# Optimization experiments

Hardware: AMD Instinct MI355X
Metric: run time of the kernel (lower is better)

The kernel has to match this reference:

```python
import jax, jax.numpy as jnp
import numpy as np

IN_FEATURES_A = 256
IN_FEATURES_B = 256


def setup_inputs() -> dict:
    key = jax.random.key(0)
    # x: [2, batch, features]; x[0] -> x_a, x[1] -> x_b
    x = jax.random.normal(key, (2, 2048, 256), dtype=jnp.float32)
    return {"x": x}


def reference(x) -> jnp.ndarray:
    # Split and truncate exactly like the torch module
    x_a = x[0][:, :IN_FEATURES_A]  # [B, A]
    x_b = x[1][:, :IN_FEATURES_B]  # [B, Kb]
    bsz = x_a.shape[0]
    # torch.kron of two 1-D vectors == flattened outer product (a-major order)
    y = jnp.einsum("ba,bk->bak", x_a, x_b).reshape(bsz, IN_FEATURES_A * IN_FEATURES_B)
    return jax.nn.softmax(y, axis=1)
```

## Files before the change

### kernel.cpp

```cpp
#include <hip/hip_runtime.h>


constexpr int FA   = 256;
constexpr int FB   = 256;
constexpr int ROWS = 2048;
constexpr int RPB  = 4;
constexpr float LOG2E = 1.4426950408889634f;

typedef float f32x4 __attribute__((ext_vector_type(4)));

__global__ __launch_bounds__(256) void krone_softmax_kernel(
    const float* __restrict__ x, float* __restrict__ out) {
  const int tid  = threadIdx.x;
  const int wid  = tid >> 6;
  const int lane = tid & 63;
  const int j    = lane * 4;
  const int row0 = blockIdx.x * RPB;

  __shared__ float sa[FA];
  __shared__ float wred[4][4];
  __shared__ float wsum[4];

  for (int r = 0; r < RPB; ++r) {
    const int row = row0 + r;
    const float* __restrict__ xa = x + (size_t)row * FA;
    const float* __restrict__ xb = x + (size_t)ROWS * FA + (size_t)row * FB;

    const float a = xa[tid];
    const float b = xb[tid];
    f32x4 b4 = *reinterpret_cast<const f32x4*>(&xb[j]);
    __syncthreads();
    sa[tid] = a;

    float maxa = a, mina = a, maxb = b, minb = b;
#pragma unroll
    for (int off = 32; off > 0; off >>= 1) {
      maxa = fmaxf(maxa, __shfl_xor(maxa, off));
      mina = fminf(mina, __shfl_xor(mina, off));
      maxb = fmaxf(maxb, __shfl_xor(maxb, off));
      minb = fminf(minb, __shfl_xor(minb, off));
    }
    if (lane == 0) {
      wred[wid][0] = maxa; wred[wid][1] = mina;
      wred[wid][2] = maxb; wred[wid][3] = minb;
    }
    __syncthreads();
    const float MA = fmaxf(fmaxf(wred[0][0], wred[1][0]), fmaxf(wred[2][0], wred[3][0]));
    const float mA = fminf(fminf(wred[0][1], wred[1][1]), fminf(wred[2][1], wred[3][1]));
    const float MB = fmaxf(fmaxf(wred[0][2], wred[1][2]), fmaxf(wred[2][2], wred[3][2]));
    const float mB = fminf(fminf(wred[0][3], wred[1][3]), fminf(wred[2][3], wred[3][3]));
    const float M = fmaxf(fmaxf(MA * MB, MA * mB), fmaxf(mA * MB, mA * mB));
    const float mM2 = -M * LOG2E;

    const float bs = b * LOG2E;
    float s0 = 0.f, s1 = 0.f, s2 = 0.f, s3 = 0.f;
#pragma unroll 4
    for (int i = 0; i < FA; i += 4) {
      s0 += __builtin_amdgcn_exp2f(fmaf(sa[i + 0], bs, mM2));
      s1 += __builtin_amdgcn_exp2f(fmaf(sa[i + 1], bs, mM2));
      s2 += __builtin_amdgcn_exp2f(fmaf(sa[i + 2], bs, mM2));
      s3 += __builtin_amdgcn_exp2f(fmaf(sa[i + 3], bs, mM2));
    }
    float s = (s0 + s1) + (s2 + s3);
#pragma unroll
    for (int off = 32; off > 0; off >>= 1) s += __shfl_xor(s, off);
    if (lane == 0) wsum[wid] = s;
    __syncthreads();
    const float sum = (wsum[0] + wsum[1]) + (wsum[2] + wsum[3]);

    const float C = mM2 - __builtin_amdgcn_logf(sum);

    f32x4 b4s = b4 * LOG2E;
    float* __restrict__ oseg =
        out + (size_t)row * (FA * FB) + wid * (64 * FB);
#pragma unroll 8
    for (int it = 0; it < 64; ++it) {
      const float av = sa[wid * 64 + it];
      f32x4 v;
      v.x = __builtin_amdgcn_exp2f(fmaf(av, b4s.x, C));
      v.y = __builtin_amdgcn_exp2f(fmaf(av, b4s.y, C));
      v.z = __builtin_amdgcn_exp2f(fmaf(av, b4s.z, C));
      v.w = __builtin_amdgcn_exp2f(fmaf(av, b4s.w, C));
      __builtin_nontemporal_store(v, reinterpret_cast<f32x4*>(&oseg[it * FB + j]));
    }
  }
}

extern "C" void kernel_launch(void* const* d_in, const int* in_sizes, int n_in,
                              void* d_out, int out_size, void* d_ws, size_t ws_size,
                              hipStream_t stream) {
  const float* x = (const float*)d_in[0];
  float* out = (float*)d_out;
  krone_softmax_kernel<<<ROWS / RPB, 256, 0, stream>>>(x, out);
}
```

Baseline: 109.4 us.

## Interleave next row's softmax denominator with current row's output stores

Each block now handles two rows. The exp-sum for the second row is computed inside the store loop of the first row, so the exp work can hide behind the memory-bound write stream. Shared-memory staging of x_a is replaced with wave shuffles, and each wave computes the global min/max redundantly, which removes a block barrier. The cost is more register pressure, more shuffle instructions, and half as many rows per block, which doubles the grid size.

```diff
diff --git a/kernel.cpp b/kernel.cpp
--- a/kernel.cpp
+++ b/kernel.cpp
@@ -4,85 +4,122 @@
 constexpr int FA   = 256;
 constexpr int FB   = 256;
 constexpr int ROWS = 2048;
-constexpr int RPB  = 4;
+constexpr int RPB  = 2;
 constexpr float LOG2E = 1.4426950408889634f;
 
 typedef float f32x4 __attribute__((ext_vector_type(4)));
 
-__global__ __launch_bounds__(256) void krone_softmax_kernel(
+__global__ __launch_bounds__(256) void krone_pipe_kernel(
     const float* __restrict__ x, float* __restrict__ out) {
   const int tid  = threadIdx.x;
   const int wid  = tid >> 6;
   const int lane = tid & 63;
-  const int j    = lane * 4;
   const int row0 = blockIdx.x * RPB;
 
-  __shared__ float sa[FA];
-  __shared__ float wred[4][4];
   __shared__ float wsum[4];
 
-  for (int r = 0; r < RPB; ++r) {
-    const int row = row0 + r;
-    const float* __restrict__ xa = x + (size_t)row * FA;
-    const float* __restrict__ xb = x + (size_t)ROWS * FA + (size_t)row * FB;
+  const float* __restrict__ xa0 = x + (size_t)row0 * FA;
+  const float* __restrict__ xb0 = x + (size_t)ROWS * FA + (size_t)row0 * FB;
+  const float* __restrict__ xa1 = xa0 + FA;
+  const float* __restrict__ xb1 = xb0 + FB;
 
-    const float a = xa[tid];
-    const float b = xb[tid];
-    f32x4 b4 = *reinterpret_cast<const f32x4*>(&xb[j]);
-    __syncthreads();
-    sa[tid] = a;
+  const float ar0 = xa0[lane], ar1 = xa0[64 + lane];
+  const float ar2 = xa0[128 + lane], ar3 = xa0[192 + lane];
+  const float aw  = xa0[wid * 64 + lane];
+  f32x4 b4        = *(const f32x4*)&xb0[lane * 4];
+  const float bc  = xb0[wid * 64 + lane];
+  const float nr0 = xa1[lane], nr1 = xa1[64 + lane];
+  const float nr2 = xa1[128 + lane], nr3 = xa1[192 + lane];
+  const float naw = xa1[wid * 64 + lane];
+  f32x4 nb4       = *(const f32x4*)&xb1[lane * 4];
+  const float nbc = xb1[wid * 64 + lane];
 
-    float maxa = a, mina = a, maxb = b, minb = b;
+#define MINMAX_M(A0, A1, A2, A3, B4, OUTM)                                    \
+  {                                                                           \
+    float mxa = fmaxf(fmaxf(A0, A1), fmaxf(A2, A3));                          \
+    float mna = fminf(fminf(A0, A1), fminf(A2, A3));                          \
+    float mxb = fmaxf(fmaxf(B4.x, B4.y), fmaxf(B4.z, B4.w));                  \
+    float mnb = fminf(fminf(B4.x, B4.y), fminf(B4.z, B4.w));                  \
+    _Pragma("unroll")                                                         \
+    for (int off = 32; off > 0; off >>= 1) {                                  \
+      mxa = fmaxf(mxa, __shfl_xor(mxa, off));                                 \
+      mna = fminf(mna, __shfl_xor(mna, off));                                 \
+      mxb = fmaxf(mxb, __shfl_xor(mxb, off));                                 \
+      mnb = fminf(mnb, __shfl_xor(mnb, off));                                 \
+    }                                                                         \
+    OUTM = fmaxf(fmaxf(mxa * mxb, mxa * mnb), fmaxf(mna * mxb, mna * mnb));   \
+  }
+
+  float M0; MINMAX_M(ar0, ar1, ar2, ar3, b4, M0);
+  const float mM2_0 = -M0 * LOG2E;
+  float M1; MINMAX_M(nr0, nr1, nr2, nr3, nb4, M1);
+  const float mM2_1 = -M1 * LOG2E;
+#undef MINMAX_M
+
+  const float bs0 = bc * LOG2E;
+  float a0 = 0.f, a1 = 0.f, a2 = 0.f, a3 = 0.f;
+#define DEN64(REG)                                                            \
+  _Pragma("unroll")                                                           \
+  for (int m = 0; m < 64; m += 4) {                                           \
+    a0 += __builtin_amdgcn_exp2f(fmaf(__shfl(REG, m + 0), bs0, mM2_0));       \
+    a1 += __builtin_amdgcn_exp2f(fmaf(__shfl(REG, m + 1), bs0, mM2_0));       \
+    a2 += __builtin_amdgcn_exp2f(fmaf(__shfl(REG, m + 2), bs0, mM2_0));       \
+    a3 += __builtin_amdgcn_exp2f(fmaf(__shfl(REG, m + 3), bs0, mM2_0));       \
+  }
+  DEN64(ar0) DEN64(ar1) DEN64(ar2) DEN64(ar3)
+#undef DEN64
+  float part = (a0 + a1) + (a2 + a3);
 #pragma unroll
-    for (int off = 32; off > 0; off >>= 1) {
-      maxa = fmaxf(maxa, __shfl_xor(maxa, off));
-      mina = fminf(mina, __shfl_xor(mina, off));
-      maxb = fmaxf(maxb, __shfl_xor(maxb, off));
-      minb = fminf(minb, __shfl_xor(minb, off));
-    }
-    if (lane == 0) {
-      wred[wid][0] = maxa; wred[wid][1] = mina;
-      wred[wid][2] = maxb; wred[wid][3] = minb;
-    }
-    __syncthreads();
-    const float MA = fmaxf(fmaxf(wred[0][0], wred[1][0]), fmaxf(wred[2][0], wred[3][0]));
-    const float mA = fminf(fminf(wred[0][1], wred[1][1]), fminf(wred[2][1], wred[3][1]));
-    const float MB = fmaxf(fmaxf(wred[0][2], wred[1][2]), fmaxf(wred[2][2], wred[3][2]));
-    const float mB = fminf(fminf(wred[0][3], wred[1][3]), fminf(wred[2][3], wred[3][3]));
-    const float M = fmaxf(fmaxf(MA * MB, MA * mB), fmaxf(mA * MB, mA * mB));
-    const float mM2 = -M * LOG2E;
+  for (int off = 32; off > 0; off >>= 1) part += __shfl_xor(part, off);
+  if (lane == 0) wsum[wid] = part;
+  __syncthreads();
+  const float sum0 = (wsum[0] + wsum[1]) + (wsum[2] + wsum[3]);
+  const float C0 = mM2_0 - __builtin_amdgcn_logf(sum0);
+  __syncthreads();
 
-    const float bs = b * LOG2E;
-    float s0 = 0.f, s1 = 0.f, s2 = 0.f, s3 = 0.f;
-#pragma unroll 4
-    for (int i = 0; i < FA; i += 4) {
-      s0 += __builtin_amdgcn_exp2f(fmaf(sa[i + 0], bs, mM2));
-      s1 += __builtin_amdgcn_exp2f(fmaf(sa[i + 1], bs, mM2));
-      s2 += __builtin_amdgcn_exp2f(fmaf(sa[i + 2], bs, mM2));
-      s3 += __builtin_amdgcn_exp2f(fmaf(sa[i + 3], bs, mM2));
-    }
-    float s = (s0 + s1) + (s2 + s3);
+  const f32x4 b4s = b4 * LOG2E;
+  const float bsn = nbc * LOG2E;
+  float* __restrict__ oseg0 = out + (size_t)row0 * (FA * FB) + wid * (64 * FB);
+  float d0 = 0.f, d1 = 0.f, d2 = 0.f, d3 = 0.f;
+#define SUBBLK(S, NREG)                                                       \
+  _Pragma("unroll")                                                           \
+  for (int k = 0; k < 16; ++k) {                                              \
+    const int it = 16 * (S) + k;                                              \
+    const float av = __shfl(aw, it);                                          \
+    f32x4 v;                                                                  \
+    v.x = __builtin_amdgcn_exp2f(fmaf(av, b4s.x, C0));                        \
+    v.y = __builtin_amdgcn_exp2f(fmaf(av, b4s.y, C0));                        \
+    v.z = __builtin_amdgcn_exp2f(fmaf(av, b4s.z, C0));                        \
+    v.w = __builtin_amdgcn_exp2f(fmaf(av, b4s.w, C0));                        \
+    __builtin_nontemporal_store(v, (f32x4*)&oseg0[it * FB + lane * 4]);       \
+    d0 += __builtin_amdgcn_exp2f(fmaf(__shfl(NREG, 4 * k + 0), bsn, mM2_1));  \
+    d1 += __builtin_amdgcn_exp2f(fmaf(__shfl(NREG, 4 * k + 1), bsn, mM2_1));  \
+    d2 += __builtin_amdgcn_exp2f(fmaf(__shfl(NREG, 4 * k + 2), bsn, mM2_1));  \
+    d3 += __builtin_amdgcn_exp2f(fmaf(__shfl(NREG, 4 * k + 3), bsn, mM2_1));  \
+  }
+  SUBBLK(0, nr0) SUBBLK(1, nr1) SUBBLK(2, nr2) SUBBLK(3, nr3)
+#undef SUBBLK
+
+  float partn = (d0 + d1) + (d2 + d3);
 #pragma unroll
-    for (int off = 32; off > 0; off >>= 1) s += __shfl_xor(s, off);
-    if (lane == 0) wsum[wid] = s;
-    __syncthreads();
-    const float sum = (wsum[0] + wsum[1]) + (wsum[2] + wsum[3]);
+  for (int off = 32; off > 0; off >>= 1) partn += __shfl_xor(partn, off);
+  if (lane == 0) wsum[wid] = partn;
+  __syncthreads();
+  const float sum1 = (wsum[0] + wsum[1]) + (wsum[2] + wsum[3]);
+  const float C1 = mM2_1 - __builtin_amdgcn_logf(sum1);
 
-    const float C = mM2 - __builtin_amdgcn_logf(sum);
-
-    f32x4 b4s = b4 * LOG2E;
-    float* __restrict__ oseg =
-        out + (size_t)row * (FA * FB) + wid * (64 * FB);
+  const f32x4 nb4s = nb4 * LOG2E;
+  float* __restrict__ oseg1 =
+      out + (size_t)(row0 + 1) * (FA * FB) + wid * (64 * FB);
 #pragma unroll 8
-    for (int it = 0; it < 64; ++it) {
-      const float av = sa[wid * 64 + it];
-      f32x4 v;
-      v.x = __builtin_amdgcn_exp2f(fmaf(av, b4s.x, C));
-      v.y = __builtin_amdgcn_exp2f(fmaf(av, b4s.y, C));
-      v.z = __builtin_amdgcn_exp2f(fmaf(av, b4s.z, C));
-      v.w = __builtin_amdgcn_exp2f(fmaf(av, b4s.w, C));
-      __builtin_nontemporal_store(v, reinterpret_cast<f32x4*>(&oseg[it * FB + j]));
-    }
+  for (int it = 0; it < 64; ++it) {
+    const float av = __shfl(naw, it);
+    f32x4 v;
+    v.x = __builtin_amdgcn_exp2f(fmaf(av, nb4s.x, C1));
+    v.y = __builtin_amdgcn_exp2f(fmaf(av, nb4s.y, C1));
+    v.z = __builtin_amdgcn_exp2f(fmaf(av, nb4s.z, C1));
+    v.w = __builtin_amdgcn_exp2f(fmaf(av, nb4s.w, C1));
+    __builtin_nontemporal_store(v, (f32x4*)&oseg1[it * FB + lane * 4]);
   }
 }
 
@@ -91,5 +128,5 @@
                               hipStream_t stream) {
   const float* x = (const float*)d_in[0];
   float* out = (float*)d_out;
-  krone_softmax_kernel<<<ROWS / RPB, 256, 0, stream>>>(x, out);
+  krone_pipe_kernel<<<ROWS / RPB, 256, 0, stream>>>(x, out);
 }
```

New measurement: 105.8 us. 3.3% less time.
